# Kernel tuning notes

Measured on AMD Instinct MI355X. Metric: run time of the kernel, lower is better.

Reference implementation:

```python
import jax, jax.numpy as jnp
import numpy as np

C = 256  # channels
SHAPES = [(8, C, 80, 80), (8, C, 40, 40), (8, C, 20, 20), (8, C, 10, 10)]
EPS = 1e-8  # torch cosine_similarity eps


def _nearest_resize(x, H, W):
    # Matches F.interpolate(mode='nearest'): src_idx = floor(dst_idx * in/out)
    b, c, h, w = x.shape
    rows = (jnp.arange(H) * h) // H
    cols = (jnp.arange(W) * w) // W
    return x[:, :, rows[:, None], cols[None, :]]


def setup_inputs() -> dict:
    key = jax.random.key(0)
    ks = jax.random.split(key, 12)
    d = {}
    for i, s in enumerate(SHAPES):
        d[f"f{i}"] = jax.random.normal(ks[i], s, dtype=jnp.float32)
        d[f"w{i}"] = jax.random.normal(ks[4 + i], (C, C), dtype=jnp.float32) / jnp.sqrt(jnp.float32(C))
        d[f"b{i}"] = jax.random.normal(ks[8 + i], (C,), dtype=jnp.float32) * 0.01
    return d


def reference(f0, f1, f2, f3, w0, w1, w2, w3, b0, b1, b2, b3):
    feats = [f0, f1, f2, f3]
    ws = [w0, w1, w2, w3]
    bs = [b0, b1, b2, b3]
    H = max(f.shape[2] for f in feats)
    W = max(f.shape[3] for f in feats)
    proj = []
    for f, w, b in zip(feats, ws, bs):
        # 1x1 conv == per-pixel GEMM over channels
        p = jnp.einsum('bchw,oc->bohw', f, w) + b[None, :, None, None]
        if p.shape[2] != H or p.shape[3] != W:
            p = _nearest_resize(p, H, W)
        proj.append(p)
    B = proj[0].shape[0]
    N = len(proj)
    x = jnp.stack(proj, axis=1).reshape(B, N, C, H * W)  # [B,N,C,L]
    # Pairwise cosine similarity along channel dim at each spatial location,
    # then mean over locations (vectorized form of the O(N^2) torch loop).
    dot = jnp.einsum('bicl,bjcl->bijl', x, x)            # [B,N,N,L]
    nrm = jnp.sqrt(jnp.einsum('bicl,bicl->bil', x, x))   # [B,N,L]
    denom = jnp.maximum(nrm[:, :, None, :] * nrm[:, None, :, :], EPS)
    attn = (dot / denom).mean(axis=-1)                   # [B,N,N]
    return jax.nn.softmax(attn, axis=-1)
```

## Files before the change

kernel.cpp:

```cpp
#include <hip/hip_runtime.h>


#define CCH 256

typedef __attribute__((ext_vector_type(8))) short short8;
typedef __attribute__((ext_vector_type(4))) short short4_;
typedef __attribute__((ext_vector_type(4))) float float4_;

__device__ inline short f2bf(float x) {
    union { float f; unsigned u; } c; c.f = x;
    unsigned u = c.u + 0x7FFFu + ((c.u >> 16) & 1u);
    return (short)(u >> 16);
}
__device__ inline float bf2f(short b) {
    union { unsigned u; float f; } c; c.u = ((unsigned)(unsigned short)b) << 16;
    return c.f;
}

__device__ inline void dma16(const void* g, void* l) {
    __builtin_amdgcn_global_load_lds(
        (const __attribute__((address_space(1))) void*)g,
        (__attribute__((address_space(3))) void*)l, 16, 0, 0);
}

__global__ __launch_bounds__(256) void pack_w(
    const float* __restrict__ w0, const float* __restrict__ w1,
    const float* __restrict__ w2, const float* __restrict__ w3,
    short* __restrict__ wp, unsigned* __restrict__ counter)
{
    if (blockIdx.x == 0 && threadIdx.x == 0) *counter = 0u;
    int id = blockIdx.x * 256 + threadIdx.x;
    int mtx = id >> 13;
    const float* w = (mtx == 0) ? w0 : (mtx == 1) ? w1 : (mtx == 2) ? w2 : w3;
    int rest = id & 8191;
    int ks = rest >> 10;
    int r2 = rest & 1023;
    int mt = r2 >> 6;
    int fl = r2 & 63;
    int ln = fl & 15, qd = fl >> 4;
    const float* src = w + (size_t)(mt * 16 + ln) * CCH + ks * 32 + qd * 8;
    short8 v;
#pragma unroll
    for (int j = 0; j < 8; ++j) v[j] = f2bf(src[j]);
    *(short8*)(wp + (size_t)id * 8) = v;
}

__global__ __launch_bounds__(256) void proj_small(
    const float* __restrict__ f1, const float* __restrict__ f2,
    const float* __restrict__ f3, const short* __restrict__ wp,
    const float* __restrict__ b1, const float* __restrict__ b2,
    const float* __restrict__ b3,
    short* __restrict__ u1, short* __restrict__ u2, short* __restrict__ u3)
{
    __shared__ __align__(16) short Wt0[16 * 512];
    __shared__ __align__(16) short Wt1[16 * 512];
    __shared__ __align__(16) short Wt2[16 * 512];
    __shared__ __align__(16) float Ft0[32 * 64];
    __shared__ __align__(16) float Ft1[32 * 64];
    __shared__ __align__(16) float Ft2[32 * 64];

    const int blk = blockIdx.x;
    const int t = threadIdx.x;

    int b, tile, L, sidx;
    const float* F; const float* bias; short* U;
    if (blk < 200)      { int r = blk;       b = r / 25; tile = r % 25; L = 1600; F = f1; bias = b1; U = u1; sidx = 1; }
    else if (blk < 256) { int r = blk - 200; b = r / 7;  tile = r % 7;  L = 400;  F = f2; bias = b2; U = u2; sidx = 2; }
    else                { int r = blk - 256; b = r / 2;  tile = r % 2;  L = 100;  F = f3; bias = b3; U = u3; sidx = 3; }

    const int lane = t & 63;
    const int wav  = t >> 6;
    const int ln   = lane & 15;
    const int quad = lane >> 4;
    const int pixbase = tile * 64;
    const float* Fb = F + (size_t)b * CCH * L;
    const short* wps = wp + (size_t)sidx * 65536;

    int gp = pixbase + (lane & 15) * 4;
    if (gp > L - 4) gp = L - 4;
    const int chq = lane >> 4;

    auto dmaW = [&](int ks, int buf) {
        short* Wb = (buf == 0) ? Wt0 : (buf == 1) ? Wt1 : Wt2;
#pragma unroll
        for (int m = 0; m < 4; ++m) {
            const int k = wav * 4 + m;
            dma16(wps + (size_t)ks * 8192 + k * 512 + lane * 8, Wb + k * 512);
        }
    };
    auto dmaF = [&](int ks, int buf) {
        float* Fl = (buf == 0) ? Ft0 : (buf == 1) ? Ft1 : Ft2;
#pragma unroll
        for (int m = 0; m < 2; ++m) {
            const int k4 = wav * 2 + m;
            const int ch = k4 * 4 + chq;
            dma16(Fb + (size_t)(ks * 32 + ch) * L + gp, Fl + k4 * 256);
        }
    };

    float4_ acc[16];
#pragma unroll
    for (int i = 0; i < 16; ++i) acc[i] = (float4_){0.f, 0.f, 0.f, 0.f};

    const int fpx = wav * 16 + ln;

    dmaW(0, 0); dmaF(0, 0);
    dmaW(1, 1); dmaF(1, 1);
#pragma unroll
    for (int ks = 0; ks < 8; ++ks) {
        if (ks < 7) asm volatile("s_waitcnt vmcnt(6)" ::: "memory");
        else        asm volatile("s_waitcnt vmcnt(0)" ::: "memory");
        __builtin_amdgcn_s_barrier();
        if (ks < 6) { dmaW(ks + 2, (ks + 2) % 3); dmaF(ks + 2, (ks + 2) % 3); }

        const short* Wl = (ks % 3 == 0) ? Wt0 : (ks % 3 == 1) ? Wt1 : Wt2;
        const float* Fl = (ks % 3 == 0) ? Ft0 : (ks % 3 == 1) ? Ft1 : Ft2;
        short8 bfrag;
#pragma unroll
        for (int j = 0; j < 8; ++j)
            bfrag[j] = f2bf(Fl[(quad * 8 + j) * 64 + fpx]);
#pragma unroll
        for (int mt = 0; mt < 16; ++mt) {
            short8 afrag = *(const short8*)(Wl + mt * 512 + lane * 8);
            acc[mt] = __builtin_amdgcn_mfma_f32_16x16x32_bf16(afrag, bfrag, acc[mt], 0, 0, 0);
        }
    }

    float ss = 0.f;
#pragma unroll
    for (int mt = 0; mt < 16; ++mt) {
        float4_ bv = *(const float4_*)(bias + mt * 16 + quad * 4);
#pragma unroll
        for (int r = 0; r < 4; ++r) { float v = acc[mt][r] + bv[r]; acc[mt][r] = v; ss += v * v; }
    }
    ss += __shfl_xor(ss, 16);
    ss += __shfl_xor(ss, 32);
    const float inv = 1.f / sqrtf(fmaxf(ss, 1e-24f));

    const int gpixw = pixbase + fpx;
    if (gpixw < L) {
        short* dst = U + ((size_t)b * L + gpixw) * CCH;
#pragma unroll
        for (int mt = 0; mt < 16; ++mt) {
            short4_ v;
#pragma unroll
            for (int r = 0; r < 4; ++r) v[r] = f2bf(acc[mt][r] * inv);
            *(short4_*)(dst + mt * 16 + quad * 4) = v;
        }
    }
}

#define SPITCH 264
__global__ __launch_bounds__(512) void proj0_dots(
    const float* __restrict__ F, const short* __restrict__ wp,
    const float* __restrict__ bias,
    const short* __restrict__ u1, const short* __restrict__ u2,
    const short* __restrict__ u3,
    float* __restrict__ partial, unsigned* __restrict__ counter,
    float* __restrict__ out)
{
    extern __shared__ __align__(16) char smem[];
    short* Wb0 = (short*)smem;
    short* Wb1 = (short*)(smem + 16384);
    short* Wb2 = (short*)(smem + 32768);
    float* Fb0 = (float*)(smem + 49152);
    float* Fb1 = (float*)(smem + 81920);
    float* Fb2 = (float*)(smem + 114688);
    short* S1 = (short*)smem;
    short* S2 = (short*)(smem + 33792);
    short* S3 = (short*)(smem + 42240);
    float* redF = (float*)(smem + 44352);
    float* redC = (float*)(smem + 44448);
    int*   lastF = (int*)(smem + 44544);

    const int c  = blockIdx.x;
    const int b  = blockIdx.y;
    const int R  = c / 5, C = c - R * 5;
    const int t  = threadIdx.x;
    const int lane = t & 63;
    const int wav  = t >> 6;
    const int ln   = lane & 15;
    const int quad = lane >> 4;
    const float* Fbase = F + (size_t)b * CCH * 6400;

    auto dmaW = [&](int ks, int buf) {
        short* Wb = (buf == 0) ? Wb0 : (buf == 1) ? Wb1 : Wb2;
#pragma unroll
        for (int m = 0; m < 2; ++m) {
            const int k = wav * 2 + m;
            dma16(wp + (size_t)ks * 8192 + k * 512 + lane * 8, Wb + k * 512);
        }
    };
    auto dmaF = [&](int ks, int buf) {
        float* Fl = (buf == 0) ? Fb0 : (buf == 1) ? Fb1 : Fb2;
        const int gpx = (16 * R + (lane >> 2)) * 80 + 16 * C + (lane & 3) * 4;
#pragma unroll
        for (int m = 0; m < 4; ++m) {
            const int k = wav * 4 + m;
            dma16(Fbase + (size_t)(ks * 32 + k) * 6400 + gpx, Fl + k * 256);
        }
    };

    float4_ accA[16], accB[16];
#pragma unroll
    for (int i = 0; i < 16; ++i) {
        accA[i] = (float4_){0.f, 0.f, 0.f, 0.f};
        accB[i] = (float4_){0.f, 0.f, 0.f, 0.f};
    }

    const int pxA = wav * 32 + ln;
    const int pxB = pxA + 16;

    dmaW(0, 0); dmaF(0, 0);
    dmaW(1, 1); dmaF(1, 1);
#pragma unroll
    for (int ks = 0; ks < 8; ++ks) {
        if (ks < 7) asm volatile("s_waitcnt vmcnt(6)" ::: "memory");
        else        asm volatile("s_waitcnt vmcnt(0)" ::: "memory");
        __builtin_amdgcn_s_barrier();
        if (ks < 6) { dmaW(ks + 2, (ks + 2) % 3); dmaF(ks + 2, (ks + 2) % 3); }

        const short* Wl = (ks % 3 == 0) ? Wb0 : (ks % 3 == 1) ? Wb1 : Wb2;
        const float* Fl = (ks % 3 == 0) ? Fb0 : (ks % 3 == 1) ? Fb1 : Fb2;
        short8 bfA, bfB;
#pragma unroll
        for (int j = 0; j < 8; ++j) {
            bfA[j] = f2bf(Fl[(quad * 8 + j) * 256 + pxA]);
            bfB[j] = f2bf(Fl[(quad * 8 + j) * 256 + pxB]);
        }
#pragma unroll
        for (int mt = 0; mt < 16; ++mt) {
            short8 afrag = *(const short8*)(Wl + mt * 512 + lane * 8);
            accA[mt] = __builtin_amdgcn_mfma_f32_16x16x32_bf16(afrag, bfA, accA[mt], 0, 0, 0);
            accB[mt] = __builtin_amdgcn_mfma_f32_16x16x32_bf16(afrag, bfB, accB[mt], 0, 0, 0);
        }
    }

    float ssA = 0.f, ssB = 0.f;
#pragma unroll
    for (int mt = 0; mt < 16; ++mt) {
        float4_ bv = *(const float4_*)(bias + mt * 16 + quad * 4);
#pragma unroll
        for (int r = 0; r < 4; ++r) {
            float vA = accA[mt][r] + bv[r]; accA[mt][r] = vA; ssA += vA * vA;
            float vB = accB[mt][r] + bv[r]; accB[mt][r] = vB; ssB += vB * vB;
        }
    }
    ssA += __shfl_xor(ssA, 16); ssA += __shfl_xor(ssA, 32);
    ssB += __shfl_xor(ssB, 16); ssB += __shfl_xor(ssB, 32);
    const float invA = 1.f / sqrtf(fmaxf(ssA, 1e-24f));
    const float invB = 1.f / sqrtf(fmaxf(ssB, 1e-24f));

    __syncthreads();

    {
        const int p1 = t >> 3, co = (t & 7) * 32;
        const int lr = p1 >> 3, lc = p1 & 7;
        const short* src = u1 + ((size_t)(b * 1600 + (8 * R + lr) * 40 + 8 * C + lc)) * CCH + co;
        short* dst = S1 + p1 * SPITCH + co;
#pragma unroll
        for (int j = 0; j < 4; ++j) *(short8*)(dst + j * 8) = *(const short8*)(src + j * 8);
    }
    if (t < 128) {
        const int p2 = t >> 3, co = (t & 7) * 32;
        const int lr = p2 >> 2, lc = p2 & 3;
        const short* src = u2 + ((size_t)(b * 400 + (4 * R + lr) * 20 + 4 * C + lc)) * CCH + co;
        short* dst = S2 + p2 * SPITCH + co;
#pragma unroll
        for (int j = 0; j < 4; ++j) *(short8*)(dst + j * 8) = *(const short8*)(src + j * 8);
    }
    if (t < 32) {
        const int p3 = t >> 3, co = (t & 7) * 32;
        const int lr = p3 >> 1, lc = p3 & 1;
        const short* src = u3 + ((size_t)(b * 100 + (2 * R + lr) * 10 + 2 * C + lc)) * CCH + co;
        short* dst = S3 + p3 * SPITCH + co;
#pragma unroll
        for (int j = 0; j < 4; ++j) *(short8*)(dst + j * 8) = *(const short8*)(src + j * 8);
    }
    __syncthreads();

    const int c1l = wav * 8 + (ln >> 1);
    const int c2l = (wav >> 1) * 4 + (ln >> 2);
    const int c3l = (wav >> 2) * 2 + (ln >> 3);
    float d01 = 0.f, d02 = 0.f, d03 = 0.f;
#pragma unroll
    for (int mt = 0; mt < 16; ++mt) {
        const int ch = mt * 16 + quad * 4;
        short4_ v1 = *(const short4_*)(&S1[c1l * SPITCH + ch]);
        short4_ v2 = *(const short4_*)(&S2[c2l * SPITCH + ch]);
        short4_ v3 = *(const short4_*)(&S3[c3l * SPITCH + ch]);
#pragma unroll
        for (int r = 0; r < 4; ++r) {
            float s = accA[mt][r] * invA + accB[mt][r] * invB;
            d01 += s * bf2f(v1[r]);
            d02 += s * bf2f(v2[r]);
            d03 += s * bf2f(v3[r]);
        }
    }
    {
        float vals[3] = {d01, d02, d03};
#pragma unroll
        for (int p = 0; p < 3; ++p) {
            float v = vals[p];
            v += __shfl_xor(v, 1);  v += __shfl_xor(v, 2);  v += __shfl_xor(v, 4);
            v += __shfl_xor(v, 8);  v += __shfl_xor(v, 16); v += __shfl_xor(v, 32);
            if (lane == 0) redF[wav * 3 + p] = v;
        }
    }

    if (wav < 4) {
        const int p1 = wav * 16 + (lane >> 2);
        const int q  = lane & 3;
        const int lr = p1 >> 3, lc = p1 & 7;
        const int par2 = (lr >> 1) * 4 + (lc >> 1);
        const int par3 = (lr >> 2) * 2 + (lc >> 2);
        float e12 = 0.f, e13 = 0.f;
#pragma unroll
        for (int k = 0; k < 16; ++k) {
            const int co = k * 16 + q * 4;
            short4_ a1 = *(const short4_*)(&S1[p1 * SPITCH + co]);
            short4_ a2 = *(const short4_*)(&S2[par2 * SPITCH + co]);
            short4_ a3 = *(const short4_*)(&S3[par3 * SPITCH + co]);
#pragma unroll
            for (int r = 0; r < 4; ++r) {
                float x1 = bf2f(a1[r]);
                e12 += x1 * bf2f(a2[r]);
                e13 += x1 * bf2f(a3[r]);
            }
        }
        float ev[2] = {e12, e13};
#pragma unroll
        for (int p = 0; p < 2; ++p) {
            float v = ev[p];
            v += __shfl_xor(v, 1);  v += __shfl_xor(v, 2);  v += __shfl_xor(v, 4);
            v += __shfl_xor(v, 8);  v += __shfl_xor(v, 16); v += __shfl_xor(v, 32);
            if (lane == 0) redC[wav * 2 + p] = v;
        }
    } else if (wav == 4) {
        const int p2 = lane >> 2;
        const int q  = lane & 3;
        const int lr = p2 >> 2, lc = p2 & 3;
        const int par3 = (lr >> 1) * 2 + (lc >> 1);
        float e23 = 0.f;
#pragma unroll
        for (int k = 0; k < 16; ++k) {
            const int co = k * 16 + q * 4;
            short4_ a2 = *(const short4_*)(&S2[p2 * SPITCH + co]);
            short4_ a3 = *(const short4_*)(&S3[par3 * SPITCH + co]);
#pragma unroll
            for (int r = 0; r < 4; ++r) e23 += bf2f(a2[r]) * bf2f(a3[r]);
        }
        e23 += __shfl_xor(e23, 1);  e23 += __shfl_xor(e23, 2);  e23 += __shfl_xor(e23, 4);
        e23 += __shfl_xor(e23, 8);  e23 += __shfl_xor(e23, 16); e23 += __shfl_xor(e23, 32);
        if (lane == 0) redC[8] = e23;
    }
    __syncthreads();

    if (t < 6) {
        float v;
        if (t < 3) {
            v = 0.f;
#pragma unroll
            for (int w = 0; w < 8; ++w) v += redF[w * 3 + t];
        } else if (t == 3) v = redC[0] + redC[2] + redC[4] + redC[6];
        else if (t == 4)   v = redC[1] + redC[3] + redC[5] + redC[7];
        else               v = redC[8];
        partial[((size_t)b * 6 + t) * 25 + c] = v;
    }

    __threadfence();
    if (t == 0) {
        unsigned old = atomicAdd(counter, 1u);
        *lastF = (old == 199u) ? 1 : 0;
    }
    __syncthreads();
    if (*lastF) {
        __threadfence();
        if (t < 128) {
            int bb = t >> 4, i = (t >> 2) & 3, j = t & 3;
            float a[4];
#pragma unroll
            for (int jj = 0; jj < 4; ++jj) {
                if (jj == i) { a[jj] = 1.0f; continue; }
                int lo = i < jj ? i : jj;
                int hi = i < jj ? jj : i;
                int pidx;
                if (lo == 0) pidx = hi - 1;
                else if (lo == 1) pidx = 1 + hi;
                else pidx = 5;
                const float* pp = partial + ((size_t)bb * 6 + pidx) * 25;
                float s = 0.f;
                for (int k = 0; k < 25; ++k) s += pp[k];
                int rf = 80 >> lo;
                a[jj] = s / (float)(rf * rf);
            }
            float m = fmaxf(fmaxf(a[0], a[1]), fmaxf(a[2], a[3]));
            float e0 = expf(a[0] - m), e1 = expf(a[1] - m), e2 = expf(a[2] - m), e3 = expf(a[3] - m);
            float sum = e0 + e1 + e2 + e3;
            float ev = (j == 0) ? e0 : (j == 1) ? e1 : (j == 2) ? e2 : e3;
            out[t] = ev / sum;
        }
    }
}

extern "C" void kernel_launch(void* const* d_in, const int* in_sizes, int n_in,
                              void* d_out, int out_size, void* d_ws, size_t ws_size,
                              hipStream_t stream) {
    const float* f[4]  = {(const float*)d_in[0], (const float*)d_in[3],
                          (const float*)d_in[6], (const float*)d_in[9]};
    const float* w[4]  = {(const float*)d_in[1], (const float*)d_in[4],
                          (const float*)d_in[7], (const float*)d_in[10]};
    const float* bs[4] = {(const float*)d_in[2], (const float*)d_in[5],
                          (const float*)d_in[8], (const float*)d_in[11]};

    char* ws = (char*)d_ws;
    size_t off = 0;
    short* u1 = (short*)(ws + off); off += (size_t)8 * CCH * 1600 * sizeof(short);
    short* u2 = (short*)(ws + off); off += (size_t)8 * CCH * 400  * sizeof(short);
    short* u3 = (short*)(ws + off); off += (size_t)8 * CCH * 100  * sizeof(short);
    short* wp = (short*)(ws + off); off += (size_t)4 * 65536 * sizeof(short);
    float* partial = (float*)(ws + off); off += (size_t)8 * 6 * 25 * sizeof(float);
    unsigned* counter = (unsigned*)(ws + off);

    static int smax_set = 0;
    if (!smax_set) {
        hipFuncSetAttribute(reinterpret_cast<const void*>(proj0_dots),
                            hipFuncAttributeMaxDynamicSharedMemorySize, 147456);
        smax_set = 1;
    }

    pack_w<<<128, 256, 0, stream>>>(w[0], w[1], w[2], w[3], wp, counter);

    proj_small<<<272, 256, 0, stream>>>(f[1], f[2], f[3], wp,
                                        bs[1], bs[2], bs[3],
                                        u1, u2, u3);

    proj0_dots<<<dim3(25, 8), 512, 147456, stream>>>(f[0], wp, bs[0],
                                                     u1, u2, u3, partial,
                                                     counter, (float*)d_out);
}
```

Baseline: 163.7 us.

## Split final softmax into its own kernel and reorder DMA prefetch after MFMAs

Removes the atomic-counter 'last block' pattern, with its thread fences and counter reset, from proj0_dots and pack_w. The final softmax now runs in a separate one-block kernel launched afterwards. In both GEMM kernels, the prefetch for stage ks+2 is now issued after the MFMA loop instead of right after the barrier. proj0_dots also gets a launch_bounds minimum of 2 blocks. The costs are an extra kernel launch, less copy/compute overlap, and a register cap under launch bounds that may cause spills.

```diff
diff --git a/kernel.cpp b/kernel.cpp
--- a/kernel.cpp
+++ b/kernel.cpp
@@ -26,9 +26,8 @@
 __global__ __launch_bounds__(256) void pack_w(
     const float* __restrict__ w0, const float* __restrict__ w1,
     const float* __restrict__ w2, const float* __restrict__ w3,
-    short* __restrict__ wp, unsigned* __restrict__ counter)
+    short* __restrict__ wp)
 {
-    if (blockIdx.x == 0 && threadIdx.x == 0) *counter = 0u;
     int id = blockIdx.x * 256 + threadIdx.x;
     int mtx = id >> 13;
     const float* w = (mtx == 0) ? w0 : (mtx == 1) ? w1 : (mtx == 2) ? w2 : w3;
@@ -111,7 +110,6 @@
         if (ks < 7) asm volatile("s_waitcnt vmcnt(6)" ::: "memory");
         else        asm volatile("s_waitcnt vmcnt(0)" ::: "memory");
         __builtin_amdgcn_s_barrier();
-        if (ks < 6) { dmaW(ks + 2, (ks + 2) % 3); dmaF(ks + 2, (ks + 2) % 3); }
 
         const short* Wl = (ks % 3 == 0) ? Wt0 : (ks % 3 == 1) ? Wt1 : Wt2;
         const float* Fl = (ks % 3 == 0) ? Ft0 : (ks % 3 == 1) ? Ft1 : Ft2;
@@ -124,6 +122,8 @@
             short8 afrag = *(const short8*)(Wl + mt * 512 + lane * 8);
             acc[mt] = __builtin_amdgcn_mfma_f32_16x16x32_bf16(afrag, bfrag, acc[mt], 0, 0, 0);
         }
+
+        if (ks < 6) { dmaW(ks + 2, (ks + 2) % 3); dmaF(ks + 2, (ks + 2) % 3); }
     }
 
     float ss = 0.f;
@@ -151,13 +151,12 @@
 }
 
 #define SPITCH 264
-__global__ __launch_bounds__(512) void proj0_dots(
+__global__ __launch_bounds__(512, 2) void proj0_dots(
     const float* __restrict__ F, const short* __restrict__ wp,
     const float* __restrict__ bias,
     const short* __restrict__ u1, const short* __restrict__ u2,
     const short* __restrict__ u3,
-    float* __restrict__ partial, unsigned* __restrict__ counter,
-    float* __restrict__ out)
+    float* __restrict__ partial)
 {
     extern __shared__ __align__(16) char smem[];
     short* Wb0 = (short*)smem;
@@ -171,7 +170,6 @@
     short* S3 = (short*)(smem + 42240);
     float* redF = (float*)(smem + 44352);
     float* redC = (float*)(smem + 44448);
-    int*   lastF = (int*)(smem + 44544);
 
     const int c  = blockIdx.x;
     const int b  = blockIdx.y;
@@ -218,7 +216,6 @@
         if (ks < 7) asm volatile("s_waitcnt vmcnt(6)" ::: "memory");
         else        asm volatile("s_waitcnt vmcnt(0)" ::: "memory");
         __builtin_amdgcn_s_barrier();
-        if (ks < 6) { dmaW(ks + 2, (ks + 2) % 3); dmaF(ks + 2, (ks + 2) % 3); }
 
         const short* Wl = (ks % 3 == 0) ? Wb0 : (ks % 3 == 1) ? Wb1 : Wb2;
         const float* Fl = (ks % 3 == 0) ? Fb0 : (ks % 3 == 1) ? Fb1 : Fb2;
@@ -234,6 +231,8 @@
             accA[mt] = __builtin_amdgcn_mfma_f32_16x16x32_bf16(afrag, bfA, accA[mt], 0, 0, 0);
             accB[mt] = __builtin_amdgcn_mfma_f32_16x16x32_bf16(afrag, bfB, accB[mt], 0, 0, 0);
         }
+
+        if (ks < 6) { dmaW(ks + 2, (ks + 2) % 3); dmaF(ks + 2, (ks + 2) % 3); }
     }
 
     float ssA = 0.f, ssB = 0.f;
@@ -367,40 +366,33 @@
         else               v = redC[8];
         partial[((size_t)b * 6 + t) * 25 + c] = v;
     }
-
-    __threadfence();
-    if (t == 0) {
-        unsigned old = atomicAdd(counter, 1u);
-        *lastF = (old == 199u) ? 1 : 0;
-    }
-    __syncthreads();
-    if (*lastF) {
-        __threadfence();
-        if (t < 128) {
-            int bb = t >> 4, i = (t >> 2) & 3, j = t & 3;
-            float a[4];
-#pragma unroll
-            for (int jj = 0; jj < 4; ++jj) {
-                if (jj == i) { a[jj] = 1.0f; continue; }
-                int lo = i < jj ? i : jj;
-                int hi = i < jj ? jj : i;
-                int pidx;
-                if (lo == 0) pidx = hi - 1;
-                else if (lo == 1) pidx = 1 + hi;
-                else pidx = 5;
-                const float* pp = partial + ((size_t)bb * 6 + pidx) * 25;
-                float s = 0.f;
-                for (int k = 0; k < 25; ++k) s += pp[k];
-                int rf = 80 >> lo;
-                a[jj] = s / (float)(rf * rf);
-            }
-            float m = fmaxf(fmaxf(a[0], a[1]), fmaxf(a[2], a[3]));
-            float e0 = expf(a[0] - m), e1 = expf(a[1] - m), e2 = expf(a[2] - m), e3 = expf(a[3] - m);
-            float sum = e0 + e1 + e2 + e3;
-            float ev = (j == 0) ? e0 : (j == 1) ? e1 : (j == 2) ? e2 : e3;
-            out[t] = ev / sum;
-        }
-    }
+}
+
+__global__ void softmax4(const float* __restrict__ partial, float* __restrict__ out) {
+    int t = threadIdx.x;
+    if (t >= 128) return;
+    int b = t >> 4, i = (t >> 2) & 3, j = t & 3;
+    float a[4];
+#pragma unroll
+    for (int jj = 0; jj < 4; ++jj) {
+        if (jj == i) { a[jj] = 1.0f; continue; }
+        int lo = i < jj ? i : jj;
+        int hi = i < jj ? jj : i;
+        int pidx;
+        if (lo == 0) pidx = hi - 1;
+        else if (lo == 1) pidx = 1 + hi;
+        else pidx = 5;
+        const float* pp = partial + ((size_t)b * 6 + pidx) * 25;
+        float s = 0.f;
+        for (int k = 0; k < 25; ++k) s += pp[k];
+        int rf = 80 >> lo;
+        a[jj] = s / (float)(rf * rf);
+    }
+    float m = fmaxf(fmaxf(a[0], a[1]), fmaxf(a[2], a[3]));
+    float e0 = expf(a[0] - m), e1 = expf(a[1] - m), e2 = expf(a[2] - m), e3 = expf(a[3] - m);
+    float sum = e0 + e1 + e2 + e3;
+    float ev = (j == 0) ? e0 : (j == 1) ? e1 : (j == 2) ? e2 : e3;
+    out[t] = ev / sum;
 }
 
 extern "C" void kernel_launch(void* const* d_in, const int* in_sizes, int n_in,
@@ -419,8 +411,7 @@
     short* u2 = (short*)(ws + off); off += (size_t)8 * CCH * 400  * sizeof(short);
     short* u3 = (short*)(ws + off); off += (size_t)8 * CCH * 100  * sizeof(short);
     short* wp = (short*)(ws + off); off += (size_t)4 * 65536 * sizeof(short);
-    float* partial = (float*)(ws + off); off += (size_t)8 * 6 * 25 * sizeof(float);
-    unsigned* counter = (unsigned*)(ws + off);
+    float* partial = (float*)(ws + off);
 
     static int smax_set = 0;
     if (!smax_set) {
@@ -429,13 +420,14 @@
         smax_set = 1;
     }
 
-    pack_w<<<128, 256, 0, stream>>>(w[0], w[1], w[2], w[3], wp, counter);
+    pack_w<<<128, 256, 0, stream>>>(w[0], w[1], w[2], w[3], wp);
 
     proj_small<<<272, 256, 0, stream>>>(f[1], f[2], f[3], wp,
                                         bs[1], bs[2], bs[3],
                                         u1, u2, u3);
 
     proj0_dots<<<dim3(25, 8), 512, 147456, stream>>>(f[0], wp, bs[0],
-                                                     u1, u2, u3, partial,
-                                                     counter, (float*)d_out);
-}
+                                                     u1, u2, u3, partial);
+
+    softmax4<<<1, 128, 0, stream>>>(partial, (float*)d_out);
+}
```

Measured after the change: 161.6 us. No clear change (-1.3%).
